# Kernel optimization log

Hardware: AMD Instinct MI355X
Metric: run time of the kernel (lower is better)

The kernel has to match this reference:

```python
import jax, jax.numpy as jnp
import numpy as np

EMBED = 1024
HEADS = 16
HEAD_DIM = EMBED // HEADS
BATCH = 2
SEQ = 256

def setup_inputs() -> dict:
    key = jax.random.key(0)
    ks = jax.random.split(key, 6)
    x = jax.random.normal(ks[0], (BATCH, SEQ, EMBED), dtype=jnp.float32)
    s = 1.0 / np.sqrt(HEAD_DIM)
    Wq = jax.random.uniform(ks[1], (HEAD_DIM, HEAD_DIM), jnp.float32, -s, s)
    Wk = jax.random.uniform(ks[2], (HEAD_DIM, HEAD_DIM), jnp.float32, -s, s)
    Wv = jax.random.uniform(ks[3], (HEAD_DIM, HEAD_DIM), jnp.float32, -s, s)
    so = 1.0 / np.sqrt(EMBED)
    Wo = jax.random.uniform(ks[4], (EMBED, EMBED), jnp.float32, -so, so)
    bo = jax.random.uniform(ks[5], (EMBED,), jnp.float32, -so, so)
    return {"x": x, "Wq": Wq, "Wk": Wk, "Wv": Wv, "Wo": Wo, "bo": bo}

def reference(x, Wq, Wk, Wv, Wo, bo):
    n, s, e = x.shape
    xr = x.reshape(n, s, HEADS, HEAD_DIM)          # (n,s,h,d)
    # nn.Linear applies x @ W.T
    q = jnp.einsum('nshd,ed->nshe', xr, Wq)
    k = jnp.einsum('nshd,ed->nshe', xr, Wk)
    v = jnp.einsum('nshd,ed->nshe', xr, Wv)
    # elementwise outer-product score: (n,s,t,h,d), no reduction over d
    energy = q[:, :, None, :, :] * k[:, None, :, :, :]
    # NOTE: original code softmaxes over dim=3 == the HEADS axis
    attn = jax.nn.softmax(energy / jnp.float32(np.sqrt(EMBED)), axis=3)
    out = jnp.einsum('nsthd,nthd->nshd', attn, v)  # reduce over t
    out = out.reshape(n, s, HEADS * HEAD_DIM)
    return out @ Wo.T + bo
```

## Files before the change

### kernel.cpp

```cpp
#include <hip/hip_runtime.h>

#define NB 2
#define SQL 256
#define NH 16
#define HD 64
#define EMB 1024

typedef unsigned short ushortT;
typedef unsigned int uintT;
typedef __attribute__((ext_vector_type(8))) short bf16x8;
typedef __attribute__((ext_vector_type(4))) float f32x4;

__device__ __constant__ float kQSCALE = 1.4426950408889634f / 32.0f;

__device__ __forceinline__ float fexp2(float x) { return __builtin_amdgcn_exp2f(x); }
__device__ __forceinline__ float frcp(float x)  { return __builtin_amdgcn_rcpf(x); }

__device__ __forceinline__ ushortT f2bf(float x) {
    uintT u = __float_as_uint(x);
    u += 0x7fffu + ((u >> 16) & 1u);
    return (ushortT)(u >> 16);
}
__device__ __forceinline__ ushort4 f2bf4(float4 a) {
    return make_ushort4(f2bf(a.x), f2bf(a.y), f2bf(a.z), f2bf(a.w));
}
__device__ __forceinline__ void unpk8(uint4 u, float* f) {
    f[0] = __uint_as_float(u.x << 16); f[1] = __uint_as_float(u.x & 0xffff0000u);
    f[2] = __uint_as_float(u.y << 16); f[3] = __uint_as_float(u.y & 0xffff0000u);
    f[4] = __uint_as_float(u.z << 16); f[5] = __uint_as_float(u.z & 0xffff0000u);
    f[6] = __uint_as_float(u.w << 16); f[7] = __uint_as_float(u.w & 0xffff0000u);
}
__device__ __forceinline__ float pairsum_dpp(float u) {
    const int j = __builtin_amdgcn_mov_dpp(__float_as_int(u), 0xB1, 0xF, 0xF, true);
    return u + __int_as_float(j);
}

__global__ __launch_bounds__(256) void qkv_kernel(
    const float* __restrict__ x,
    const float* __restrict__ Wq,
    const float* __restrict__ Wk,
    const float* __restrict__ Wv,
    const float* __restrict__ Wo,
    const float* __restrict__ bo,
    ushortT* __restrict__ Q,
    ushortT* __restrict__ K,
    ushortT* __restrict__ V,
    float* __restrict__ AO,
    float* __restrict__ out,
    ushortT* __restrict__ Wob)
{
    __shared__ ushortT wls[3][64 * 72];
    __shared__ ushortT xs[2][16 * 72];

    const int tid = threadIdx.x;
    const int ns0 = blockIdx.x * 2;
    const int g   = blockIdx.x * 256 + tid;

    {
        const float4 z = make_float4(0.f, 0.f, 0.f, 0.f);
        ((float4*)AO)[g] = z;
        ((float4*)AO)[g + 65536] = z;
        const float4 bb = ((const float4*)bo)[g & 255];
        ((float4*)out)[g] = bb;
        ((float4*)out)[g + 65536] = bb;
    }
#pragma unroll
    for (int j = 0; j < 4; ++j) {
        const int f4 = j * 65536 + g;
        ((ushort4*)Wob)[f4] = f2bf4(((const float4*)Wo)[f4]);
    }

#pragma unroll
    for (int m = 0; m < 3; ++m) {
        const float4* src = (m == 0) ? (const float4*)Wq
                          : (m == 1) ? (const float4*)Wk : (const float4*)Wv;
#pragma unroll
        for (int j = 0; j < 4; ++j) {
            const int idx = j * 256 + tid;
            const int e   = idx >> 4;
            const int d4  = idx & 15;
            float4 a = src[idx];
            if (m == 0) { a.x *= kQSCALE; a.y *= kQSCALE; a.z *= kQSCALE; a.w *= kQSCALE; }
            *(ushort4*)&wls[m][e * 72 + d4 * 4] = f2bf4(a);
        }
    }
#pragma unroll
    for (int j = 0; j < 2; ++j) {
        const int idx = j * 256 + tid;
        const int r   = idx >> 8;
        const int h   = (idx >> 4) & 15;
        const int d4  = idx & 15;
        const float4 a = ((const float4*)(x + (size_t)(ns0 + r) * EMB))[idx & 255];
        *(ushort4*)&xs[r][h * 72 + d4 * 4] = f2bf4(a);
    }
    __syncthreads();

    const int w   = tid >> 6;
    const int nsr = w >> 1;
    const int eb0 = (w & 1) * 32;
    const int l   = tid & 63;
    const int lr  = l & 15;
    const int lk  = l >> 4;

    const bf16x8 a0 = *(const bf16x8*)&xs[nsr][lr * 72 + lk * 8];
    const bf16x8 a1 = *(const bf16x8*)&xs[nsr][lr * 72 + 32 + lk * 8];

#pragma unroll
    for (int m = 0; m < 3; ++m) {
        ushortT* outp = (m == 0) ? Q : (m == 1) ? K : V;
#pragma unroll
        for (int ef = 0; ef < 2; ++ef) {
            const int eb = eb0 + ef * 16;
            const bf16x8 b0 = *(const bf16x8*)&wls[m][(eb + lr) * 72 + lk * 8];
            const bf16x8 b1 = *(const bf16x8*)&wls[m][(eb + lr) * 72 + 32 + lk * 8];
            f32x4 c = {0.f, 0.f, 0.f, 0.f};
            c = __builtin_amdgcn_mfma_f32_16x16x32_bf16(a0, b0, c, 0, 0, 0);
            c = __builtin_amdgcn_mfma_f32_16x16x32_bf16(a1, b1, c, 0, 0, 0);
            ushortT* dst = outp + (size_t)(ns0 + nsr) * EMB + (eb + lr) * 16 + lk * 4;
            *(ushort4*)dst = make_ushort4(f2bf(c[0]), f2bf(c[1]), f2bf(c[2]), f2bf(c[3]));
        }
    }
}

#define ATTN_STEP(KU4, VU4)                                                    \
    {                                                                          \
        float ku[8], vu[8], p0[8], p1[8];                                      \
        unpk8(KU4, ku);                                                        \
        _Pragma("unroll")                                                      \
        for (int i = 0; i < 8; ++i) p0[i] = fexp2(qa0[i] * ku[i]);             \
        _Pragma("unroll")                                                      \
        for (int i = 0; i < 8; ++i) p1[i] = fexp2(qa1[i] * ku[i]);             \
        float u0 = ((p0[0]+p0[1]) + (p0[2]+p0[3])) + ((p0[4]+p0[5]) + (p0[6]+p0[7])); \
        float u1 = ((p1[0]+p1[1]) + (p1[2]+p1[3])) + ((p1[4]+p1[5]) + (p1[6]+p1[7])); \
        const float rs0 = frcp(pairsum_dpp(u0));                               \
        const float rs1 = frcp(pairsum_dpp(u1));                               \
        unpk8(VU4, vu);                                                        \
        _Pragma("unroll")                                                      \
        for (int i = 0; i < 8; ++i) {                                          \
            a0[i] = fmaf(p0[i] * rs0, vu[i], a0[i]);                           \
            a1[i] = fmaf(p1[i] * rs1, vu[i], a1[i]);                           \
        }                                                                      \
    }

__global__ __launch_bounds__(256) void attn_kernel(
    const ushortT* __restrict__ Q,
    const ushortT* __restrict__ K,
    const ushortT* __restrict__ V,
    float* __restrict__ AO)
{
    const int b    = blockIdx.x;
    const int tc   = b & 15;
    const int eh   = (b >> 4) & 1;
    const int st   = (b >> 5) & 31;
    const int n    = b >> 10;
    const int wave = threadIdx.x >> 6;
    const int l    = threadIdx.x & 63;
    const int s0   = st * 8 + wave * 2;
    const int t0   = tc * 16;

    float qa0[8], qa1[8];
    {
        const uint4* qp = (const uint4*)(Q + (size_t)(n * SQL + s0) * EMB + 512 * eh) + l;
        unpk8(qp[0], qa0);
        unpk8(qp[128], qa1);
    }

    float a0[8], a1[8];
#pragma unroll
    for (int i = 0; i < 8; ++i) { a0[i] = 0.f; a1[i] = 0.f; }

    const uint4* kp = (const uint4*)(K + (size_t)(n * SQL + t0) * EMB + 512 * eh) + l;
    const uint4* vp = (const uint4*)(V + (size_t)(n * SQL + t0) * EMB + 512 * eh) + l;

    uint4 ka = kp[0];
    uint4 kb = kp[128];
    uint4 va = vp[0];

#pragma unroll
    for (int tt = 0; tt < 16; tt += 2) {
        const uint4 kn2 = kp[256];
        const uint4 vb  = vp[128];
        ATTN_STEP(ka, va);
        const uint4 kn3 = kp[384];
        va = vp[256];
        kp += 256; vp += 256;
        ATTN_STEP(kb, vb);
        ka = kn2; kb = kn3;
    }

    float* base0 = AO + (size_t)(n * SQL + s0) * EMB + 512 * (l & 1) + 32 * eh + (l >> 1);
    float* base1 = base0 + EMB;
#pragma unroll
    for (int c = 0; c < 8; ++c) {
        atomicAdd(base0 + 64 * c, a0[c]);
        atomicAdd(base1 + 64 * c, a1[c]);
    }
}

__global__ __launch_bounds__(512) void proj_kernel(
    const float* __restrict__ AO,
    const ushortT* __restrict__ Wob,
    float* __restrict__ out)
{
    __shared__ ushortT As[64 * 40];
    __shared__ ushortT Bs[128 * 40];

    const int b  = blockIdx.x;
    const int kc = b & 3;
    const int jt = (b >> 2) & 7;
    const int rt = b >> 5;
    const int tid = threadIdx.x;
    const int r0 = rt * 64, j0 = jt * 128, k0 = kc * 256;

    const int w  = tid >> 6;
    const int wr = w >> 2;
    const int wc = w & 3;
    const int l  = tid & 63;
    const int lr = l & 15;
    const int lk = l >> 4;

    f32x4 c00 = {0.f, 0.f, 0.f, 0.f};
    f32x4 c01 = {0.f, 0.f, 0.f, 0.f};
    f32x4 c10 = {0.f, 0.f, 0.f, 0.f};
    f32x4 c11 = {0.f, 0.f, 0.f, 0.f};

    for (int kt = 0; kt < 8; ++kt) {
        const int kb = k0 + kt * 32;
        __syncthreads();
        {
            const int row = tid >> 3;
            const int kq  = tid & 7;
            const float4 a = *(const float4*)&AO[(size_t)(r0 + row) * EMB + kb + kq * 4];
            *(ushort4*)&As[row * 40 + kq * 4] = f2bf4(a);
        }
        {
            const int row = tid >> 2;
            const int ko  = tid & 3;
            const uint4 wv = *(const uint4*)&Wob[(size_t)(j0 + row) * EMB + kb + ko * 8];
            *(uint4*)&Bs[row * 40 + ko * 8] = wv;
        }
        __syncthreads();

        const bf16x8 a0 = *(const bf16x8*)&As[(wr * 32 + lr) * 40 + lk * 8];
        const bf16x8 a1 = *(const bf16x8*)&As[(wr * 32 + 16 + lr) * 40 + lk * 8];
        const bf16x8 b0 = *(const bf16x8*)&Bs[(wc * 32 + lr) * 40 + lk * 8];
        const bf16x8 b1 = *(const bf16x8*)&Bs[(wc * 32 + 16 + lr) * 40 + lk * 8];
        c00 = __builtin_amdgcn_mfma_f32_16x16x32_bf16(a0, b0, c00, 0, 0, 0);
        c01 = __builtin_amdgcn_mfma_f32_16x16x32_bf16(a0, b1, c01, 0, 0, 0);
        c10 = __builtin_amdgcn_mfma_f32_16x16x32_bf16(a1, b0, c10, 0, 0, 0);
        c11 = __builtin_amdgcn_mfma_f32_16x16x32_bf16(a1, b1, c11, 0, 0, 0);
    }

    const int rbase = r0 + wr * 32 + lk * 4;
    const int jbase = j0 + wc * 32 + lr;
#pragma unroll
    for (int e = 0; e < 4; ++e) {
        atomicAdd(&out[(size_t)(rbase + e) * EMB + jbase],           c00[e]);
        atomicAdd(&out[(size_t)(rbase + e) * EMB + jbase + 16],      c01[e]);
        atomicAdd(&out[(size_t)(rbase + 16 + e) * EMB + jbase],      c10[e]);
        atomicAdd(&out[(size_t)(rbase + 16 + e) * EMB + jbase + 16], c11[e]);
    }
}

extern "C" void kernel_launch(void* const* d_in, const int* in_sizes, int n_in,
                              void* d_out, int out_size, void* d_ws, size_t ws_size,
                              hipStream_t stream)
{
    const float* x  = (const float*)d_in[0];
    const float* Wq = (const float*)d_in[1];
    const float* Wk = (const float*)d_in[2];
    const float* Wv = (const float*)d_in[3];
    const float* Wo = (const float*)d_in[4];
    const float* bo = (const float*)d_in[5];

    float* ws = (float*)d_ws;
    ushortT* Q   = (ushortT*)ws;
    ushortT* K   = (ushortT*)(ws + 262144);
    ushortT* V   = (ushortT*)(ws + 524288);
    float*   AO  = ws + 786432;
    ushortT* Wob = (ushortT*)(ws + 1310720);

    qkv_kernel<<<256, 256, 0, stream>>>(x, Wq, Wk, Wv, Wo, bo, Q, K, V, AO,
                                        (float*)d_out, Wob);
    attn_kernel<<<2048, 256, 0, stream>>>(Q, K, V, AO);
    proj_kernel<<<256, 512, 0, stream>>>(AO, Wob, (float*)d_out);
}
```

Before: 59.70 us.

## Process four query rows per wave in attention with packed float2 math

Each wave now handles four query rows instead of two, so every loaded K/V vector is reused across more rows and the grid is halved. The arithmetic is rewritten with two-float vectors so the compiler can emit packed FMA and multiply instructions, and launch bounds request higher occupancy. The trade-off is higher register pressure from the larger accumulator and query arrays, and fewer blocks to spread across the GPU.

```diff
diff --git a/kernel.cpp b/kernel.cpp
--- a/kernel.cpp
+++ b/kernel.cpp
@@ -10,6 +10,7 @@
 typedef unsigned int uintT;
 typedef __attribute__((ext_vector_type(8))) short bf16x8;
 typedef __attribute__((ext_vector_type(4))) float f32x4;
+typedef __attribute__((ext_vector_type(2))) float f32x2;
 
 __device__ __constant__ float kQSCALE = 1.4426950408889634f / 32.0f;
 
@@ -24,11 +25,11 @@
 __device__ __forceinline__ ushort4 f2bf4(float4 a) {
     return make_ushort4(f2bf(a.x), f2bf(a.y), f2bf(a.z), f2bf(a.w));
 }
-__device__ __forceinline__ void unpk8(uint4 u, float* f) {
-    f[0] = __uint_as_float(u.x << 16); f[1] = __uint_as_float(u.x & 0xffff0000u);
-    f[2] = __uint_as_float(u.y << 16); f[3] = __uint_as_float(u.y & 0xffff0000u);
-    f[4] = __uint_as_float(u.z << 16); f[5] = __uint_as_float(u.z & 0xffff0000u);
-    f[6] = __uint_as_float(u.w << 16); f[7] = __uint_as_float(u.w & 0xffff0000u);
+__device__ __forceinline__ f32x2 unpk2(uintT u) {
+    f32x2 r;
+    r.x = __uint_as_float(u << 16);
+    r.y = __uint_as_float(u & 0xffff0000u);
+    return r;
 }
 __device__ __forceinline__ float pairsum_dpp(float u) {
     const int j = __builtin_amdgcn_mov_dpp(__float_as_int(u), 0xB1, 0xF, 0xF, true);
@@ -122,27 +123,32 @@
     }
 }
 
-#define ATTN_STEP(KU4, VU4)                                                    \
+#define ATTN_STEP4(KU4, VU4)                                                   \
     {                                                                          \
-        float ku[8], vu[8], p0[8], p1[8];                                      \
-        unpk8(KU4, ku);                                                        \
+        f32x2 ku[4], vu[4];                                                    \
+        ku[0] = unpk2(KU4.x); ku[1] = unpk2(KU4.y);                            \
+        ku[2] = unpk2(KU4.z); ku[3] = unpk2(KU4.w);                            \
+        vu[0] = unpk2(VU4.x); vu[1] = unpk2(VU4.y);                            \
+        vu[2] = unpk2(VU4.z); vu[3] = unpk2(VU4.w);                            \
         _Pragma("unroll")                                                      \
-        for (int i = 0; i < 8; ++i) p0[i] = fexp2(qa0[i] * ku[i]);             \
-        _Pragma("unroll")                                                      \
-        for (int i = 0; i < 8; ++i) p1[i] = fexp2(qa1[i] * ku[i]);             \
-        float u0 = ((p0[0]+p0[1]) + (p0[2]+p0[3])) + ((p0[4]+p0[5]) + (p0[6]+p0[7])); \
-        float u1 = ((p1[0]+p1[1]) + (p1[2]+p1[3])) + ((p1[4]+p1[5]) + (p1[6]+p1[7])); \
-        const float rs0 = frcp(pairsum_dpp(u0));                               \
-        const float rs1 = frcp(pairsum_dpp(u1));                               \
-        unpk8(VU4, vu);                                                        \
-        _Pragma("unroll")                                                      \
-        for (int i = 0; i < 8; ++i) {                                          \
-            a0[i] = fmaf(p0[i] * rs0, vu[i], a0[i]);                           \
-            a1[i] = fmaf(p1[i] * rs1, vu[i], a1[i]);                           \
+        for (int m = 0; m < 4; ++m) {                                          \
+            f32x2 p[4];                                                        \
+            _Pragma("unroll")                                                  \
+            for (int j = 0; j < 4; ++j) {                                      \
+                const f32x2 xq = q2[m][j] * ku[j];                             \
+                p[j].x = fexp2(xq.x);                                          \
+                p[j].y = fexp2(xq.y);                                          \
+            }                                                                  \
+            const f32x2 s = (p[0] + p[1]) + (p[2] + p[3]);                     \
+            const float rs = frcp(pairsum_dpp(s.x + s.y));                     \
+            const f32x2 rb = {rs, rs};                                         \
+            _Pragma("unroll")                                                  \
+            for (int j = 0; j < 4; ++j)                                        \
+                acc[m][j] = __builtin_elementwise_fma(vu[j] * rb, p[j], acc[m][j]); \
         }                                                                      \
     }
 
-__global__ __launch_bounds__(256) void attn_kernel(
+__global__ __launch_bounds__(256, 4) void attn_kernel(
     const ushortT* __restrict__ Q,
     const ushortT* __restrict__ K,
     const ushortT* __restrict__ V,
@@ -151,49 +157,54 @@
     const int b    = blockIdx.x;
     const int tc   = b & 15;
     const int eh   = (b >> 4) & 1;
-    const int st   = (b >> 5) & 31;
-    const int n    = b >> 10;
+    const int sg   = (b >> 5) & 15;
+    const int n    = b >> 9;
     const int wave = threadIdx.x >> 6;
     const int l    = threadIdx.x & 63;
-    const int s0   = st * 8 + wave * 2;
+    const int s0   = sg * 16 + wave * 4;
     const int t0   = tc * 16;
 
-    float qa0[8], qa1[8];
+    f32x2 q2[4][4];
     {
         const uint4* qp = (const uint4*)(Q + (size_t)(n * SQL + s0) * EMB + 512 * eh) + l;
-        unpk8(qp[0], qa0);
-        unpk8(qp[128], qa1);
-    }
-
-    float a0[8], a1[8];
-#pragma unroll
-    for (int i = 0; i < 8; ++i) { a0[i] = 0.f; a1[i] = 0.f; }
+#pragma unroll
+        for (int m = 0; m < 4; ++m) {
+            const uint4 qa = qp[m * 128];
+            q2[m][0] = unpk2(qa.x); q2[m][1] = unpk2(qa.y);
+            q2[m][2] = unpk2(qa.z); q2[m][3] = unpk2(qa.w);
+        }
+    }
+
+    f32x2 acc[4][4];
+#pragma unroll
+    for (int m = 0; m < 4; ++m)
+#pragma unroll
+        for (int j = 0; j < 4; ++j) acc[m][j] = (f32x2){0.f, 0.f};
 
     const uint4* kp = (const uint4*)(K + (size_t)(n * SQL + t0) * EMB + 512 * eh) + l;
     const uint4* vp = (const uint4*)(V + (size_t)(n * SQL + t0) * EMB + 512 * eh) + l;
 
-    uint4 ka = kp[0];
-    uint4 kb = kp[128];
-    uint4 va = vp[0];
+    uint4 ka = kp[0], va = vp[0];
+    uint4 kb = kp[128], vb = vp[128];
 
 #pragma unroll
     for (int tt = 0; tt < 16; tt += 2) {
-        const uint4 kn2 = kp[256];
-        const uint4 vb  = vp[128];
-        ATTN_STEP(ka, va);
-        const uint4 kn3 = kp[384];
-        va = vp[256];
+        ATTN_STEP4(ka, va);
+        ka = kp[256]; va = vp[256];
+        ATTN_STEP4(kb, vb);
+        kb = kp[384]; vb = vp[384];
         kp += 256; vp += 256;
-        ATTN_STEP(kb, vb);
-        ka = kn2; kb = kn3;
-    }
-
-    float* base0 = AO + (size_t)(n * SQL + s0) * EMB + 512 * (l & 1) + 32 * eh + (l >> 1);
-    float* base1 = base0 + EMB;
-#pragma unroll
-    for (int c = 0; c < 8; ++c) {
-        atomicAdd(base0 + 64 * c, a0[c]);
-        atomicAdd(base1 + 64 * c, a1[c]);
+    }
+
+    float* base = AO + (size_t)(n * SQL + s0) * EMB + 512 * (l & 1) + 32 * eh + (l >> 1);
+#pragma unroll
+    for (int m = 0; m < 4; ++m) {
+        float* bm = base + (size_t)m * EMB;
+#pragma unroll
+        for (int j = 0; j < 4; ++j) {
+            atomicAdd(bm + 64 * (2 * j),     acc[m][j].x);
+            atomicAdd(bm + 64 * (2 * j + 1), acc[m][j].y);
+        }
     }
 }
 
@@ -282,6 +293,6 @@
 
     qkv_kernel<<<256, 256, 0, stream>>>(x, Wq, Wk, Wv, Wo, bo, Q, K, V, AO,
                                         (float*)d_out, Wob);
-    attn_kernel<<<2048, 256, 0, stream>>>(Q, K, V, AO);
+    attn_kernel<<<1024, 256, 0, stream>>>(Q, K, V, AO);
     proj_kernel<<<256, 512, 0, stream>>>(AO, Wob, (float*)d_out);
 }
```

New measurement: 64.14 us. 1.07x slower.
